# Optimization experiments

Measured on AMD Instinct MI355X. Metric: run time of the kernel, lower is better.

## Reference

```python
import jax, jax.numpy as jnp
import numpy as np

N = 50000      # nodes
E = 800000     # directed edges (before self-loops)
FEAT = 120     # raw node feature dim
TOPO = 8       # topological feature dim
H1, D1 = 8, 8  # conv1: heads, per-head dim
C = 40         # out_channels (classes)
NEG_SLOPE = 0.2


def setup_inputs() -> dict:
    key = jax.random.key(0)
    ks = jax.random.split(key, 10)
    return {
        "x": jax.random.normal(ks[0], (N, FEAT), dtype=jnp.float32),
        "topo": jax.random.normal(ks[1], (N, TOPO), dtype=jnp.float32),
        "edge_index": jax.random.randint(ks[2], (2, E), 0, N, dtype=jnp.int32),
        "W1": jax.random.normal(ks[3], (FEAT + TOPO, H1 * D1), dtype=jnp.float32) * 0.1,
        "a_src1": jax.random.normal(ks[4], (H1, D1), dtype=jnp.float32) * 0.1,
        "a_dst1": jax.random.normal(ks[5], (H1, D1), dtype=jnp.float32) * 0.1,
        "b1": jnp.zeros((H1 * D1,), dtype=jnp.float32),
        "W2": jax.random.normal(ks[6], (H1 * D1, C), dtype=jnp.float32) * 0.1,
        "a_src2": jax.random.normal(ks[7], (1, C), dtype=jnp.float32) * 0.1,
        "a_dst2": jax.random.normal(ks[8], (1, C), dtype=jnp.float32) * 0.1,
        "b2": jnp.zeros((C,), dtype=jnp.float32),
    }


def gat_conv(x, src, dst, W, a_src, a_dst, b, heads, d, concat):
    """PyG-style GATConv (eval mode). src/dst already include self-loops."""
    n = x.shape[0]
    h = (x @ W).reshape(n, heads, d)                      # [N,H,D]
    al_src = jnp.sum(h * a_src[None], axis=-1)            # [N,H]
    al_dst = jnp.sum(h * a_dst[None], axis=-1)            # [N,H]
    e = jax.nn.leaky_relu(al_src[src] + al_dst[dst], NEG_SLOPE)  # [E',H]
    # segment softmax over incoming edges per destination node
    m = jax.ops.segment_max(e, dst, num_segments=n)       # [N,H]
    p = jnp.exp(e - m[dst])                               # [E',H]
    s = jax.ops.segment_sum(p, dst, num_segments=n)       # [N,H]
    alpha = p / s[dst]                                    # [E',H]
    out = jax.ops.segment_sum(alpha[:, :, None] * h[src], dst, num_segments=n)  # [N,H,D]
    if concat:
        return out.reshape(n, heads * d) + b
    return out.mean(axis=1) + b


def reference(x, topo, edge_index, W1, a_src1, a_dst1, b1, W2, a_src2, a_dst2, b2):
    n = x.shape[0]
    loops = jnp.arange(n, dtype=edge_index.dtype)
    src = jnp.concatenate([edge_index[0], loops])
    dst = jnp.concatenate([edge_index[1], loops])
    xin = jnp.concatenate([x, topo], axis=1)              # [N, FEAT+TOPO]
    h = jax.nn.elu(gat_conv(xin, src, dst, W1, a_src1, a_dst1, b1, H1, D1, True))
    out = gat_conv(h, src, dst, W2, a_src2, a_dst2, b2, 1, C, False)
    return jax.nn.log_softmax(out, axis=1)
```

## Files before the change

### kernel.cpp

```cpp
#include <hip/hip_runtime.h>
#include <hip/hip_fp16.h>

#define NN 50000
#define EE 800000
#define NBUCK 196
#define CAP 5120
#define TILEA 2048
#define NBA ((EE + TILEA - 1) / TILEA)
#define NGB 782
#define SRCS_MAX (EE + 8 * NN)

typedef _Float16 half8 __attribute__((ext_vector_type(8)));
typedef float floatx4 __attribute__((ext_vector_type(4)));
typedef float floatx2 __attribute__((ext_vector_type(2)));

__device__ __forceinline__ unsigned char f32_to_fp8(float a) {
    int r = __builtin_amdgcn_cvt_pk_fp8_f32(a, a, 0, false);
    return (unsigned char)(r & 0xff);
}
__device__ __forceinline__ float2 fp8pair_to_f32(unsigned v) {
    floatx2 r = __builtin_amdgcn_cvt_pk_f32_fp8(v, false);
    return make_float2(r[0], r[1]);
}

__global__ void k_prep(const float* __restrict__ W1, const float* __restrict__ W2,
                       _Float16* __restrict__ Bf1, _Float16* __restrict__ Bf2,
                       int* __restrict__ cursor, float* __restrict__ alsrc,
                       float* __restrict__ al2s) {
    int tid = blockIdx.x * 256 + threadIdx.x;
    if (tid < 1024) {
        int kk = tid >> 8, ct = (tid >> 6) & 3, L = tid & 63;
        int k0 = kk * 32 + (L >> 4) * 8, col = ct * 16 + (L & 15);
        half8 v;
        #pragma unroll
        for (int j = 0; j < 8; j++) v[j] = (_Float16)W1[(k0 + j) * 64 + col];
        *(half8*)(Bf1 + ((size_t)((kk * 4 + ct) * 64 + L)) * 8) = v;
    } else if (tid < 1024 + 384) {
        int u = tid - 1024;
        int kk = u / 192, rem = u % 192;
        int ct = rem >> 6, L = rem & 63;
        int k0 = kk * 32 + (L >> 4) * 8, col = ct * 16 + (L & 15);
        half8 v;
        #pragma unroll
        for (int j = 0; j < 8; j++)
            v[j] = (col < 40) ? (_Float16)W2[(k0 + j) * 40 + col] : (_Float16)0.f;
        *(half8*)(Bf2 + ((size_t)((kk * 3 + ct) * 64 + L)) * 8) = v;
    } else {
        int u = tid - 1408;
        if (u < NBUCK) cursor[u] = 0;
        if (u >= 200 && u < 208) alsrc[(size_t)NN * 8 + (u - 200)] = -1e30f;
        if (u == 208) al2s[NN] = -1e30f;
    }
}

__global__ __launch_bounds__(256) void k_fusedAG(
    const int* __restrict__ ei, int* __restrict__ cursor,
    unsigned* __restrict__ bucketData,
    const float* __restrict__ x, const float* __restrict__ topo,
    const _Float16* __restrict__ Bf1,
    const float* __restrict__ a_src, const float* __restrict__ a_dst,
    unsigned char* __restrict__ h1, float* __restrict__ alsrc, float* __restrict__ aldst) {
    if (blockIdx.x < NBA) {
        __shared__ int cnt[NBUCK], base[NBUCK];
        int t = threadIdx.x;
        for (int i = t; i < NBUCK; i += 256) cnt[i] = 0;
        __syncthreads();
        int e0 = blockIdx.x * TILEA;
        int nE = min(TILEA, EE - e0);
        unsigned pk[8]; int bk[8], rk[8];
        int m = 0;
        for (int i = t; i < nE; i += 256) {
            int e = e0 + i;
            int s = ei[e], d = ei[EE + e];
            pk[m] = ((unsigned)d << 16) | (unsigned)s;
            bk[m] = d >> 8;
            rk[m] = atomicAdd(&cnt[bk[m]], 1);
            m++;
        }
        __syncthreads();
        for (int i = t; i < NBUCK; i += 256)
            base[i] = (cnt[i] > 0) ? atomicAdd(&cursor[i], cnt[i]) : 0;
        __syncthreads();
        for (int k = 0; k < m; k++) {
            int pos = base[bk[k]] + rk[k];
            if (pos < CAP) bucketData[(size_t)bk[k] * CAP + pos] = pk[k];
        }
        return;
    }
    int wave = threadIdx.x >> 6, lane = threadIdx.x & 63;
    int row0 = (blockIdx.x - NBA) * 64 + wave * 16;
    if (row0 >= NN) return;
    int g = lane >> 4, li = lane & 15;
    int myrow = row0 + li;
    half8 B[16];
    const half8* bp = (const half8*)Bf1;
    #pragma unroll
    for (int i = 0; i < 16; i++) B[i] = bp[i * 64 + lane];
    floatx4 acc[4] = {{0,0,0,0},{0,0,0,0},{0,0,0,0},{0,0,0,0}};
    #pragma unroll
    for (int kk = 0; kk < 4; kk++) {
        int k0 = kk * 32 + g * 8;
        const float* sp = (k0 == 120) ? (topo + (size_t)myrow * 8)
                                      : (x + (size_t)myrow * 120 + k0);
        float4 u0 = ((const float4*)sp)[0];
        float4 u1 = ((const float4*)sp)[1];
        half8 av;
        av[0] = (_Float16)u0.x; av[1] = (_Float16)u0.y;
        av[2] = (_Float16)u0.z; av[3] = (_Float16)u0.w;
        av[4] = (_Float16)u1.x; av[5] = (_Float16)u1.y;
        av[6] = (_Float16)u1.z; av[7] = (_Float16)u1.w;
        #pragma unroll
        for (int ct = 0; ct < 4; ct++)
            acc[ct] = __builtin_amdgcn_mfma_f32_16x16x32_f16(av, B[kk * 4 + ct], acc[ct], 0, 0, 0);
    }
    #pragma unroll
    for (int ct = 0; ct < 4; ct++)
        #pragma unroll
        for (int r = 0; r < 4; r++)
            h1[(size_t)(row0 + 4 * g + r) * 64 + ct * 16 + li] = f32_to_fp8(acc[ct][r]);
    float ps[4][4], pd[4][4];
    #pragma unroll
    for (int ct = 0; ct < 4; ct++) {
        int head = 2 * ct + (li >> 3), dix = li & 7;
        float asv = a_src[head * 8 + dix];
        float adv = a_dst[head * 8 + dix];
        #pragma unroll
        for (int r = 0; r < 4; r++) {
            ps[ct][r] = acc[ct][r] * asv;
            pd[ct][r] = acc[ct][r] * adv;
        }
    }
    #pragma unroll
    for (int off = 1; off <= 4; off <<= 1)
        #pragma unroll
        for (int ct = 0; ct < 4; ct++)
            #pragma unroll
            for (int r = 0; r < 4; r++) {
                ps[ct][r] += __shfl_xor(ps[ct][r], off, 64);
                pd[ct][r] += __shfl_xor(pd[ct][r], off, 64);
            }
    if ((li & 7) == 0) {
        #pragma unroll
        for (int ct = 0; ct < 4; ct++) {
            int head = 2 * ct + (li >> 3);
            #pragma unroll
            for (int r = 0; r < 4; r++) {
                int row = row0 + 4 * g + r;
                alsrc[row * 8 + head] = ps[ct][r];
                aldst[row * 8 + head] = pd[ct][r];
            }
        }
    }
}

__global__ __launch_bounds__(1024) void k_bucketB(const unsigned* __restrict__ bucketData,
        const int* __restrict__ cursor,
        int2* __restrict__ rowseg, int* __restrict__ srcs) {
    __shared__ int cnt[256], cur[256], sbuf[256], svals[256];
    __shared__ int sorted[CAP + 2048];
    int b = blockIdx.x, t = threadIdx.x;
    int nloc = min(256, NN - b * 256);
    int ecnt = min(cursor[b], CAP);
    size_t inBase = (size_t)b * CAP;
    if (t < 256) {
        int vv = 0;
        if (t < NBUCK) {
            int nl = min(256, NN - t * 256);
            vv = min(cursor[t], CAP) + 8 * nl;
        }
        svals[t] = vv;
    }
    __syncthreads();
    int* a = svals; int* bb = sbuf;
    for (int off = 1; off < 256; off <<= 1) {
        if (t < 256) bb[t] = a[t] + ((t >= off) ? a[t - off] : 0);
        __syncthreads();
        int* tmp = a; a = bb; bb = tmp;
    }
    int outBase = (b == 0) ? 0 : a[b - 1];
    __syncthreads();
    if (t < 256) cnt[t] = (t < nloc) ? 1 : 0;
    __syncthreads();
    for (int i = t; i < ecnt; i += 1024) {
        unsigned u = bucketData[inBase + i];
        atomicAdd(&cnt[(u >> 16) & 255], 1);
    }
    __syncthreads();
    int cv = 0, pcv = 0;
    if (t < 256) {
        cv = cnt[t];
        pcv = (t < nloc) ? ((cv + 7) & ~7) : 0;
        sbuf[t] = pcv;
    }
    __syncthreads();
    a = sbuf; bb = cnt;
    for (int off = 1; off < 256; off <<= 1) {
        if (t < 256) bb[t] = a[t] + ((t >= off) ? a[t - off] : 0);
        __syncthreads();
        int* tmp = a; a = bb; bb = tmp;
    }
    int total = a[255];
    int excl = (t < 256) ? (a[t] - pcv) : 0;
    __syncthreads();
    if (t < nloc) {
        rowseg[b * 256 + t] = make_int2(outBase + excl, outBase + excl + pcv);
        sorted[excl] = b * 256 + t;
        for (int k = cv; k < pcv; k++) sorted[excl + k] = NN;
        cur[t] = excl + 1;
    }
    __syncthreads();
    for (int i = t; i < ecnt; i += 1024) {
        unsigned u = bucketData[inBase + i];
        int ld = (u >> 16) & 255;
        int p = atomicAdd(&cur[ld], 1);
        sorted[p] = (int)(u & 0xffffu);
    }
    __syncthreads();
    for (int i = t; i < total; i += 1024) srcs[outBase + i] = sorted[i];
}

__global__ __launch_bounds__(256) void k_agg1(
    const int2* __restrict__ rowseg, const int* __restrict__ srcs,
    const float* __restrict__ alsrc, const float* __restrict__ aldst,
    const unsigned char* __restrict__ h1, const float* __restrict__ b1,
    __half* __restrict__ hout) {
    int wave = threadIdx.x >> 6;
    int lane = threadIdx.x & 63;
    int d = blockIdx.x * 4 + wave;
    if (d >= NN) return;
    int hs = lane >> 5;
    int cp = lane & 31;
    int hh = cp >> 2;
    float adst = aldst[d * 8 + hh];
    int2 seg = rowseg[d];
    int jb = seg.x, je = seg.y;
    float ssum = 0.f, ax = 0.f, ay = 0.f;
    int sA0 = srcs[jb + hs],     sA1 = srcs[jb + 2 + hs];
    int sA2 = srcs[jb + 4 + hs], sA3 = srcs[jb + 6 + hs];
    for (int j = jb; j < je; j += 8) {
        int s0 = sA0, s1 = sA1, s2 = sA2, s3 = sA3;
        int jn = j + 8;
        if (jn < je) {
            sA0 = srcs[jn + hs];     sA1 = srcs[jn + 2 + hs];
            sA2 = srcs[jn + 4 + hs]; sA3 = srcs[jn + 6 + hs];
        }
        float e0 = alsrc[s0 * 8 + hh] + adst;
        float e1 = alsrc[s1 * 8 + hh] + adst;
        float e2 = alsrc[s2 * 8 + hh] + adst;
        float e3 = alsrc[s3 * 8 + hh] + adst;
        unsigned q0 = *(const unsigned short*)(h1 + (size_t)s0 * 64 + 2 * cp);
        unsigned q1 = *(const unsigned short*)(h1 + (size_t)s1 * 64 + 2 * cp);
        unsigned q2 = *(const unsigned short*)(h1 + (size_t)s2 * 64 + 2 * cp);
        unsigned q3 = *(const unsigned short*)(h1 + (size_t)s3 * 64 + 2 * cp);
        float p0 = __expf(fmaxf(e0, 0.2f * e0));
        float p1 = __expf(fmaxf(e1, 0.2f * e1));
        float p2 = __expf(fmaxf(e2, 0.2f * e2));
        float p3 = __expf(fmaxf(e3, 0.2f * e3));
        float2 f0 = fp8pair_to_f32(q0), f1 = fp8pair_to_f32(q1);
        float2 f2 = fp8pair_to_f32(q2), f3 = fp8pair_to_f32(q3);
        ssum += (p0 + p1) + (p2 + p3);
        ax += p0 * f0.x + p1 * f1.x + p2 * f2.x + p3 * f3.x;
        ay += p0 * f0.y + p1 * f1.y + p2 * f2.y + p3 * f3.y;
    }
    ssum += __shfl_xor(ssum, 32, 64);
    ax += __shfl_xor(ax, 32, 64);
    ay += __shfl_xor(ay, 32, 64);
    if (hs == 0) {
        float2 bv = *(const float2*)(b1 + 2 * cp);
        float inv = 1.f / ssum;
        float vx = ax * inv + bv.x;
        float vy = ay * inv + bv.y;
        vx = (vx > 0.f) ? vx : (__expf(vx) - 1.f);
        vy = (vy > 0.f) ? vy : (__expf(vy) - 1.f);
        *(__half2*)(hout + (size_t)d * 64 + 2 * cp) = __floats2half2_rn(vx, vy);
    }
}

__global__ __launch_bounds__(256) void k_gemm2(
    const __half* __restrict__ hout, const _Float16* __restrict__ Bf2,
    const float* __restrict__ a_src2, const float* __restrict__ a_dst2,
    __half* __restrict__ h2, float* __restrict__ al2s, float* __restrict__ al2d) {
    int wave = threadIdx.x >> 6, lane = threadIdx.x & 63;
    int row0 = blockIdx.x * 64 + wave * 16;
    if (row0 >= NN) return;
    int g = lane >> 4, li = lane & 15;
    int myrow = row0 + li;
    half8 B[6];
    const half8* bp = (const half8*)Bf2;
    #pragma unroll
    for (int i = 0; i < 6; i++) B[i] = bp[i * 64 + lane];
    floatx4 acc[3] = {{0,0,0,0},{0,0,0,0},{0,0,0,0}};
    #pragma unroll
    for (int kk = 0; kk < 2; kk++) {
        int k0 = kk * 32 + g * 8;
        half8 av = *(const half8*)(hout + (size_t)myrow * 64 + k0);
        #pragma unroll
        for (int ct = 0; ct < 3; ct++)
            acc[ct] = __builtin_amdgcn_mfma_f32_16x16x32_f16(av, B[kk * 3 + ct], acc[ct], 0, 0, 0);
    }
    float ts[4] = {0.f, 0.f, 0.f, 0.f}, td[4] = {0.f, 0.f, 0.f, 0.f};
    #pragma unroll
    for (int ct = 0; ct < 3; ct++) {
        int col = ct * 16 + li;
        bool ok = (col < 40);
        float asv = ok ? a_src2[col] : 0.f;
        float adv = ok ? a_dst2[col] : 0.f;
        #pragma unroll
        for (int r = 0; r < 4; r++) {
            ts[r] += acc[ct][r] * asv;
            td[r] += acc[ct][r] * adv;
            if (ok) h2[(size_t)(row0 + 4 * g + r) * 40 + col] = __float2half(acc[ct][r]);
        }
    }
    #pragma unroll
    for (int off = 1; off <= 8; off <<= 1)
        #pragma unroll
        for (int r = 0; r < 4; r++) {
            ts[r] += __shfl_xor(ts[r], off, 64);
            td[r] += __shfl_xor(td[r], off, 64);
        }
    if (li == 0) {
        #pragma unroll
        for (int r = 0; r < 4; r++) {
            int row = row0 + 4 * g + r;
            al2s[row] = ts[r];
            al2d[row] = td[r];
        }
    }
}

__global__ __launch_bounds__(256) void k_agg2(
    const int2* __restrict__ rowseg, const int* __restrict__ srcs,
    const float* __restrict__ al2s, const float* __restrict__ al2d,
    const __half* __restrict__ h2, const float* __restrict__ b2,
    float* __restrict__ out) {
    int wave = threadIdx.x >> 6;
    int lane = threadIdx.x & 63;
    int d = blockIdx.x * 4 + wave;
    if (d >= NN) return;
    int hs = lane >> 5;
    int cp = lane & 31;
    bool act = (cp < 20);
    int cpc = act ? cp : 0;
    float adst = al2d[d];
    int2 seg = rowseg[d];
    int jb = seg.x, je = seg.y;
    float ssum = 0.f, ax = 0.f, ay = 0.f;
    int sA0 = srcs[jb + hs],     sA1 = srcs[jb + 2 + hs];
    int sA2 = srcs[jb + 4 + hs], sA3 = srcs[jb + 6 + hs];
    for (int j = jb; j < je; j += 8) {
        int s0 = sA0, s1 = sA1, s2 = sA2, s3 = sA3;
        int jn = j + 8;
        if (jn < je) {
            sA0 = srcs[jn + hs];     sA1 = srcs[jn + 2 + hs];
            sA2 = srcs[jn + 4 + hs]; sA3 = srcs[jn + 6 + hs];
        }
        float e0 = al2s[s0] + adst;
        float e1 = al2s[s1] + adst;
        float e2 = al2s[s2] + adst;
        float e3 = al2s[s3] + adst;
        __half2 v0 = *(const __half2*)(h2 + (size_t)s0 * 40 + 2 * cpc);
        __half2 v1 = *(const __half2*)(h2 + (size_t)s1 * 40 + 2 * cpc);
        __half2 v2 = *(const __half2*)(h2 + (size_t)s2 * 40 + 2 * cpc);
        __half2 v3 = *(const __half2*)(h2 + (size_t)s3 * 40 + 2 * cpc);
        float p0 = __expf(fmaxf(e0, 0.2f * e0));
        float p1 = __expf(fmaxf(e1, 0.2f * e1));
        float p2 = __expf(fmaxf(e2, 0.2f * e2));
        float p3 = __expf(fmaxf(e3, 0.2f * e3));
        float2 f0 = __half22float2(v0), f1 = __half22float2(v1);
        float2 f2 = __half22float2(v2), f3 = __half22float2(v3);
        ssum += (p0 + p1) + (p2 + p3);
        ax += p0 * f0.x + p1 * f1.x + p2 * f2.x + p3 * f3.x;
        ay += p0 * f0.y + p1 * f1.y + p2 * f2.y + p3 * f3.y;
    }
    ssum += __shfl_xor(ssum, 32, 64);
    ax += __shfl_xor(ax, 32, 64);
    ay += __shfl_xor(ay, 32, 64);
    float inv = 1.f / ssum;
    float2 bv = *(const float2*)(b2 + 2 * cpc);
    float ox = ax * inv + bv.x;
    float oy = ay * inv + bv.y;
    float mo = act ? fmaxf(ox, oy) : -3.0e38f;
    #pragma unroll
    for (int off = 16; off; off >>= 1) mo = fmaxf(mo, __shfl_xor(mo, off, 64));
    float te = act ? (__expf(ox - mo) + __expf(oy - mo)) : 0.f;
    #pragma unroll
    for (int off = 16; off; off >>= 1) te += __shfl_xor(te, off, 64);
    float ls = __logf(te);
    if (act && hs == 0)
        *(float2*)(out + (size_t)d * 40 + 2 * cp) = make_float2(ox - mo - ls, oy - mo - ls);
}

extern "C" void kernel_launch(void* const* d_in, const int* in_sizes, int n_in,
                              void* d_out, int out_size, void* d_ws, size_t ws_size,
                              hipStream_t stream) {
    (void)in_sizes; (void)n_in; (void)out_size; (void)ws_size;
    const float* x    = (const float*)d_in[0];
    const float* topo = (const float*)d_in[1];
    const int*   ei   = (const int*)d_in[2];
    const float* W1   = (const float*)d_in[3];
    const float* as1  = (const float*)d_in[4];
    const float* ad1  = (const float*)d_in[5];
    const float* b1   = (const float*)d_in[6];
    const float* W2   = (const float*)d_in[7];
    const float* as2  = (const float*)d_in[8];
    const float* ad2  = (const float*)d_in[9];
    const float* b2   = (const float*)d_in[10];
    float* out = (float*)d_out;

    char* ws = (char*)d_ws;
    size_t off = 0;
    auto alloc = [&](size_t bytes) {
        void* p = ws + off;
        off += (bytes + 255) / 256 * 256;
        return p;
    };
    int2*          rowseg     = (int2*)alloc((size_t)NN * 8);
    int*           cursor     = (int*)alloc(NBUCK * 4);
    unsigned*      bucketData = (unsigned*)alloc((size_t)NBUCK * CAP * 4);
    int*           srcs       = (int*)alloc((size_t)SRCS_MAX * 4);
    float*         alsrc1     = (float*)alloc((size_t)(NN + 1) * 8 * 4);
    float*         aldst1     = (float*)alloc((size_t)NN * 8 * 4);
    float*         al2s       = (float*)alloc((NN + 1) * 4);
    float*         al2d       = (float*)alloc(NN * 4);
    _Float16*      Bf1        = (_Float16*)alloc(4 * 4 * 64 * 8 * 2);
    _Float16*      Bf2        = (_Float16*)alloc(2 * 3 * 64 * 8 * 2);
    unsigned char* h1         = (unsigned char*)alloc((size_t)(NN + 1) * 64);
    __half*        hout       = (__half*)alloc((size_t)NN * 64 * 2);
    __half*        h2         = (__half*)alloc((size_t)(NN + 1) * 40 * 2);

    k_prep    <<<7,         256,  0, stream>>>(W1, W2, Bf1, Bf2, cursor, alsrc1, al2s);
    k_fusedAG <<<NBA + NGB, 256,  0, stream>>>(ei, cursor, bucketData,
                                               x, topo, Bf1, as1, ad1, h1, alsrc1, aldst1);
    k_bucketB <<<NBUCK,     1024, 0, stream>>>(bucketData, cursor, rowseg, srcs);
    k_agg1    <<<(NN + 3) / 4, 256, 0, stream>>>(rowseg, srcs, alsrc1, aldst1, h1, b1, hout);
    k_gemm2   <<<782,       256,  0, stream>>>(hout, Bf2, as2, ad2, h2, al2s, al2d);
    k_agg2    <<<(NN + 3) / 4, 256, 0, stream>>>(rowseg, srcs, al2s, al2d, h2, b2, out);
}
```

Measured before the change: 172.3 us.

## Fuse layer-2 linear transform into layer-1 aggregation kernel via per-wave MFMA

```diff
diff --git a/kernel.cpp b/kernel.cpp
--- a/kernel.cpp
+++ b/kernel.cpp
@@ -13,6 +13,7 @@
 typedef _Float16 half8 __attribute__((ext_vector_type(8)));
 typedef float floatx4 __attribute__((ext_vector_type(4)));
 typedef float floatx2 __attribute__((ext_vector_type(2)));
+typedef int intx4 __attribute__((ext_vector_type(4)));
 
 __device__ __forceinline__ unsigned char f32_to_fp8(float a) {
     int r = __builtin_amdgcn_cvt_pk_fp8_f32(a, a, 0, false);
@@ -219,11 +220,13 @@
     for (int i = t; i < total; i += 1024) srcs[outBase + i] = sorted[i];
 }
 
-__global__ __launch_bounds__(256) void k_agg1(
+__global__ __launch_bounds__(256) void k_agg1g2(
     const int2* __restrict__ rowseg, const int* __restrict__ srcs,
     const float* __restrict__ alsrc, const float* __restrict__ aldst,
     const unsigned char* __restrict__ h1, const float* __restrict__ b1,
-    __half* __restrict__ hout) {
+    const _Float16* __restrict__ Bf2,
+    const float* __restrict__ a_src2, const float* __restrict__ a_dst2,
+    __half* __restrict__ h2, float* __restrict__ al2s, float* __restrict__ al2d) {
     int wave = threadIdx.x >> 6;
     int lane = threadIdx.x & 63;
     int d = blockIdx.x * 4 + wave;
@@ -265,67 +268,48 @@
     ssum += __shfl_xor(ssum, 32, 64);
     ax += __shfl_xor(ax, 32, 64);
     ay += __shfl_xor(ay, 32, 64);
-    if (hs == 0) {
-        float2 bv = *(const float2*)(b1 + 2 * cp);
-        float inv = 1.f / ssum;
-        float vx = ax * inv + bv.x;
-        float vy = ay * inv + bv.y;
-        vx = (vx > 0.f) ? vx : (__expf(vx) - 1.f);
-        vy = (vy > 0.f) ? vy : (__expf(vy) - 1.f);
-        *(__half2*)(hout + (size_t)d * 64 + 2 * cp) = __floats2half2_rn(vx, vy);
-    }
-}
-
-__global__ __launch_bounds__(256) void k_gemm2(
-    const __half* __restrict__ hout, const _Float16* __restrict__ Bf2,
-    const float* __restrict__ a_src2, const float* __restrict__ a_dst2,
-    __half* __restrict__ h2, float* __restrict__ al2s, float* __restrict__ al2d) {
-    int wave = threadIdx.x >> 6, lane = threadIdx.x & 63;
-    int row0 = blockIdx.x * 64 + wave * 16;
-    if (row0 >= NN) return;
+    float2 bv = *(const float2*)(b1 + 2 * cp);
+    float inv = 1.f / ssum;
+    float vx = ax * inv + bv.x;
+    float vy = ay * inv + bv.y;
+    vx = (vx > 0.f) ? vx : (__expf(vx) - 1.f);
+    vy = (vy > 0.f) ? vy : (__expf(vy) - 1.f);
+    __half2 hp = __floats2half2_rn(vx, vy);
+    int ph = *(int*)&hp;
     int g = lane >> 4, li = lane & 15;
-    int myrow = row0 + li;
-    half8 B[6];
-    const half8* bp = (const half8*)Bf2;
-    #pragma unroll
-    for (int i = 0; i < 6; i++) B[i] = bp[i * 64 + lane];
-    floatx4 acc[3] = {{0,0,0,0},{0,0,0,0},{0,0,0,0}};
-    #pragma unroll
-    for (int kk = 0; kk < 2; kk++) {
-        int k0 = kk * 32 + g * 8;
-        half8 av = *(const half8*)(hout + (size_t)myrow * 64 + k0);
-        #pragma unroll
-        for (int ct = 0; ct < 3; ct++)
-            acc[ct] = __builtin_amdgcn_mfma_f32_16x16x32_f16(av, B[kk * 3 + ct], acc[ct], 0, 0, 0);
-    }
-    float ts[4] = {0.f, 0.f, 0.f, 0.f}, td[4] = {0.f, 0.f, 0.f, 0.f};
-    #pragma unroll
-    for (int ct = 0; ct < 3; ct++) {
-        int col = ct * 16 + li;
-        bool ok = (col < 40);
-        float asv = ok ? a_src2[col] : 0.f;
-        float adv = ok ? a_dst2[col] : 0.f;
-        #pragma unroll
-        for (int r = 0; r < 4; r++) {
-            ts[r] += acc[ct][r] * asv;
-            td[r] += acc[ct][r] * adv;
-            if (ok) h2[(size_t)(row0 + 4 * g + r) * 40 + col] = __float2half(acc[ct][r]);
-        }
-    }
-    #pragma unroll
-    for (int off = 1; off <= 8; off <<= 1)
-        #pragma unroll
-        for (int r = 0; r < 4; r++) {
-            ts[r] += __shfl_xor(ts[r], off, 64);
-            td[r] += __shfl_xor(td[r], off, 64);
-        }
-    if (li == 0) {
-        #pragma unroll
-        for (int r = 0; r < 4; r++) {
-            int row = row0 + 4 * g + r;
-            al2s[row] = ts[r];
-            al2d[row] = td[r];
-        }
+    intx4 i0, i1;
+    #pragma unroll
+    for (int i = 0; i < 4; i++) {
+        i0[i] = __shfl(ph, (g << 2) | i, 64);
+        i1[i] = __shfl(ph, 16 + ((g << 2) | i), 64);
+    }
+    half8 av0 = __builtin_bit_cast(half8, i0);
+    half8 av1 = __builtin_bit_cast(half8, i1);
+    const half8* bp2 = (const half8*)Bf2;
+    floatx4 c0 = {0,0,0,0}, c1 = {0,0,0,0}, c2 = {0,0,0,0};
+    c0 = __builtin_amdgcn_mfma_f32_16x16x32_f16(av0, bp2[0 * 64 + lane], c0, 0, 0, 0);
+    c0 = __builtin_amdgcn_mfma_f32_16x16x32_f16(av1, bp2[3 * 64 + lane], c0, 0, 0, 0);
+    c1 = __builtin_amdgcn_mfma_f32_16x16x32_f16(av0, bp2[1 * 64 + lane], c1, 0, 0, 0);
+    c1 = __builtin_amdgcn_mfma_f32_16x16x32_f16(av1, bp2[4 * 64 + lane], c1, 0, 0, 0);
+    c2 = __builtin_amdgcn_mfma_f32_16x16x32_f16(av0, bp2[2 * 64 + lane], c2, 0, 0, 0);
+    c2 = __builtin_amdgcn_mfma_f32_16x16x32_f16(av1, bp2[5 * 64 + lane], c2, 0, 0, 0);
+    float h20 = c0[0], h21 = c1[0], h22 = c2[0];
+    float as0 = a_src2[li], ad0 = a_dst2[li];
+    float as1 = a_src2[16 + li], ad1 = a_dst2[16 + li];
+    float as2 = (li < 8) ? a_src2[32 + li] : 0.f;
+    float ad2 = (li < 8) ? a_dst2[32 + li] : 0.f;
+    float ts = h20 * as0 + h21 * as1 + h22 * as2;
+    float td = h20 * ad0 + h21 * ad1 + h22 * ad2;
+    #pragma unroll
+    for (int off = 1; off <= 8; off <<= 1) {
+        ts += __shfl_xor(ts, off, 64);
+        td += __shfl_xor(td, off, 64);
+    }
+    if (lane == 0) { al2s[d] = ts; al2d[d] = td; }
+    if (lane < 16) {
+        h2[(size_t)d * 40 + li] = __float2half(h20);
+        h2[(size_t)d * 40 + 16 + li] = __float2half(h21);
+        if (li < 8) h2[(size_t)d * 40 + 32 + li] = __float2half(h22);
     }
 }
 
@@ -426,14 +410,13 @@
     _Float16*      Bf1        = (_Float16*)alloc(4 * 4 * 64 * 8 * 2);
     _Float16*      Bf2        = (_Float16*)alloc(2 * 3 * 64 * 8 * 2);
     unsigned char* h1         = (unsigned char*)alloc((size_t)(NN + 1) * 64);
-    __half*        hout       = (__half*)alloc((size_t)NN * 64 * 2);
     __half*        h2         = (__half*)alloc((size_t)(NN + 1) * 40 * 2);
 
     k_prep    <<<7,         256,  0, stream>>>(W1, W2, Bf1, Bf2, cursor, alsrc1, al2s);
     k_fusedAG <<<NBA + NGB, 256,  0, stream>>>(ei, cursor, bucketData,
                                                x, topo, Bf1, as1, ad1, h1, alsrc1, aldst1);
     k_bucketB <<<NBUCK,     1024, 0, stream>>>(bucketData, cursor, rowseg, srcs);
-    k_agg1    <<<(NN + 3) / 4, 256, 0, stream>>>(rowseg, srcs, alsrc1, aldst1, h1, b1, hout);
-    k_gemm2   <<<782,       256,  0, stream>>>(hout, Bf2, as2, ad2, h2, al2s, al2d);
+    k_agg1g2  <<<(NN + 3) / 4, 256, 0, stream>>>(rowseg, srcs, alsrc1, aldst1, h1, b1,
+                                                 Bf2, as2, ad2, h2, al2s, al2d);
     k_agg2    <<<(NN + 3) / 4, 256, 0, stream>>>(rowseg, srcs, al2s, al2d, h2, b2, out);
 }
```

After: 176.2 us. 2.2% more time.

## Widen per-lane gathers in both aggregation kernels and pad h2 rows to 64

Applied to the files above, without the earlier changes.

```diff
diff --git a/kernel.cpp b/kernel.cpp
--- a/kernel.cpp
+++ b/kernel.cpp
@@ -18,15 +18,20 @@
     int r = __builtin_amdgcn_cvt_pk_fp8_f32(a, a, 0, false);
     return (unsigned char)(r & 0xff);
 }
-__device__ __forceinline__ float2 fp8pair_to_f32(unsigned v) {
+__device__ __forceinline__ float2 fp8pair_lo(unsigned v) {
     floatx2 r = __builtin_amdgcn_cvt_pk_f32_fp8(v, false);
+    return make_float2(r[0], r[1]);
+}
+__device__ __forceinline__ float2 fp8pair_hi(unsigned v) {
+    floatx2 r = __builtin_amdgcn_cvt_pk_f32_fp8(v, true);
     return make_float2(r[0], r[1]);
 }
 
 __global__ void k_prep(const float* __restrict__ W1, const float* __restrict__ W2,
                        _Float16* __restrict__ Bf1, _Float16* __restrict__ Bf2,
                        int* __restrict__ cursor, float* __restrict__ alsrc,
-                       float* __restrict__ al2s) {
+                       float* __restrict__ al2s, unsigned char* __restrict__ h1,
+                       __half* __restrict__ h2p) {
     int tid = blockIdx.x * 256 + threadIdx.x;
     if (tid < 1024) {
         int kk = tid >> 8, ct = (tid >> 6) & 3, L = tid & 63;
@@ -50,6 +55,8 @@
         if (u < NBUCK) cursor[u] = 0;
         if (u >= 200 && u < 208) alsrc[(size_t)NN * 8 + (u - 200)] = -1e30f;
         if (u == 208) al2s[NN] = -1e30f;
+        if (u >= 224 && u < 240) ((unsigned*)(h1 + (size_t)NN * 64))[u - 224] = 0u;
+        if (u >= 240 && u < 272) ((unsigned*)(h2p + (size_t)NN * 64))[u - 240] = 0u;
     }
 }
 
@@ -228,58 +235,62 @@
     int lane = threadIdx.x & 63;
     int d = blockIdx.x * 4 + wave;
     if (d >= NN) return;
-    int hs = lane >> 5;
-    int cp = lane & 31;
-    int hh = cp >> 2;
+    int eh = lane >> 4;
+    int cq = lane & 15;
+    int hh = cq >> 1;
     float adst = aldst[d * 8 + hh];
     int2 seg = rowseg[d];
     int jb = seg.x, je = seg.y;
-    float ssum = 0.f, ax = 0.f, ay = 0.f;
-    int sA0 = srcs[jb + hs],     sA1 = srcs[jb + 2 + hs];
-    int sA2 = srcs[jb + 4 + hs], sA3 = srcs[jb + 6 + hs];
+    float a0 = 0.f, a1 = 0.f, a2 = 0.f, a3 = 0.f, ssum = 0.f;
+    int sA = srcs[jb + eh], sB = srcs[jb + 4 + eh];
     for (int j = jb; j < je; j += 8) {
-        int s0 = sA0, s1 = sA1, s2 = sA2, s3 = sA3;
+        int s0 = sA, s1 = sB;
         int jn = j + 8;
         if (jn < je) {
-            sA0 = srcs[jn + hs];     sA1 = srcs[jn + 2 + hs];
-            sA2 = srcs[jn + 4 + hs]; sA3 = srcs[jn + 6 + hs];
+            sA = srcs[jn + eh]; sB = srcs[jn + 4 + eh];
         }
         float e0 = alsrc[s0 * 8 + hh] + adst;
         float e1 = alsrc[s1 * 8 + hh] + adst;
-        float e2 = alsrc[s2 * 8 + hh] + adst;
-        float e3 = alsrc[s3 * 8 + hh] + adst;
-        unsigned q0 = *(const unsigned short*)(h1 + (size_t)s0 * 64 + 2 * cp);
-        unsigned q1 = *(const unsigned short*)(h1 + (size_t)s1 * 64 + 2 * cp);
-        unsigned q2 = *(const unsigned short*)(h1 + (size_t)s2 * 64 + 2 * cp);
-        unsigned q3 = *(const unsigned short*)(h1 + (size_t)s3 * 64 + 2 * cp);
+        unsigned q0 = *(const unsigned*)(h1 + (size_t)s0 * 64 + 4 * cq);
+        unsigned q1 = *(const unsigned*)(h1 + (size_t)s1 * 64 + 4 * cq);
         float p0 = __expf(fmaxf(e0, 0.2f * e0));
         float p1 = __expf(fmaxf(e1, 0.2f * e1));
-        float p2 = __expf(fmaxf(e2, 0.2f * e2));
-        float p3 = __expf(fmaxf(e3, 0.2f * e3));
-        float2 f0 = fp8pair_to_f32(q0), f1 = fp8pair_to_f32(q1);
-        float2 f2 = fp8pair_to_f32(q2), f3 = fp8pair_to_f32(q3);
-        ssum += (p0 + p1) + (p2 + p3);
-        ax += p0 * f0.x + p1 * f1.x + p2 * f2.x + p3 * f3.x;
-        ay += p0 * f0.y + p1 * f1.y + p2 * f2.y + p3 * f3.y;
-    }
-    ssum += __shfl_xor(ssum, 32, 64);
-    ax += __shfl_xor(ax, 32, 64);
-    ay += __shfl_xor(ay, 32, 64);
-    if (hs == 0) {
-        float2 bv = *(const float2*)(b1 + 2 * cp);
+        float2 f0l = fp8pair_lo(q0), f0h = fp8pair_hi(q0);
+        float2 f1l = fp8pair_lo(q1), f1h = fp8pair_hi(q1);
+        ssum += p0 + p1;
+        a0 += p0 * f0l.x + p1 * f1l.x;
+        a1 += p0 * f0l.y + p1 * f1l.y;
+        a2 += p0 * f0h.x + p1 * f1h.x;
+        a3 += p0 * f0h.y + p1 * f1h.y;
+    }
+    a0 += __shfl_xor(a0, 16, 64); a0 += __shfl_xor(a0, 32, 64);
+    a1 += __shfl_xor(a1, 16, 64); a1 += __shfl_xor(a1, 32, 64);
+    a2 += __shfl_xor(a2, 16, 64); a2 += __shfl_xor(a2, 32, 64);
+    a3 += __shfl_xor(a3, 16, 64); a3 += __shfl_xor(a3, 32, 64);
+    ssum += __shfl_xor(ssum, 16, 64); ssum += __shfl_xor(ssum, 32, 64);
+    if (eh == 0) {
+        float4 bv = ((const float4*)b1)[cq];
         float inv = 1.f / ssum;
-        float vx = ax * inv + bv.x;
-        float vy = ay * inv + bv.y;
-        vx = (vx > 0.f) ? vx : (__expf(vx) - 1.f);
-        vy = (vy > 0.f) ? vy : (__expf(vy) - 1.f);
-        *(__half2*)(hout + (size_t)d * 64 + 2 * cp) = __floats2half2_rn(vx, vy);
+        float v0 = a0 * inv + bv.x;
+        float v1 = a1 * inv + bv.y;
+        float v2 = a2 * inv + bv.z;
+        float v3 = a3 * inv + bv.w;
+        v0 = (v0 > 0.f) ? v0 : (__expf(v0) - 1.f);
+        v1 = (v1 > 0.f) ? v1 : (__expf(v1) - 1.f);
+        v2 = (v2 > 0.f) ? v2 : (__expf(v2) - 1.f);
+        v3 = (v3 > 0.f) ? v3 : (__expf(v3) - 1.f);
+        __half2 h01 = __floats2half2_rn(v0, v1);
+        __half2 h23 = __floats2half2_rn(v2, v3);
+        uint2 pk;
+        pk.x = *(unsigned*)&h01; pk.y = *(unsigned*)&h23;
+        *(uint2*)(hout + (size_t)d * 64 + 4 * cq) = pk;
     }
 }
 
 __global__ __launch_bounds__(256) void k_gemm2(
     const __half* __restrict__ hout, const _Float16* __restrict__ Bf2,
     const float* __restrict__ a_src2, const float* __restrict__ a_dst2,
-    __half* __restrict__ h2, float* __restrict__ al2s, float* __restrict__ al2d) {
+    __half* __restrict__ h2p, float* __restrict__ al2s, float* __restrict__ al2d) {
     int wave = threadIdx.x >> 6, lane = threadIdx.x & 63;
     int row0 = blockIdx.x * 64 + wave * 16;
     if (row0 >= NN) return;
@@ -309,9 +320,12 @@
         for (int r = 0; r < 4; r++) {
             ts[r] += acc[ct][r] * asv;
             td[r] += acc[ct][r] * adv;
-            if (ok) h2[(size_t)(row0 + 4 * g + r) * 40 + col] = __float2half(acc[ct][r]);
-        }
-    }
+            h2p[(size_t)(row0 + 4 * g + r) * 64 + col] = __float2half(acc[ct][r]);
+        }
+    }
+    #pragma unroll
+    for (int r = 0; r < 4; r++)
+        h2p[(size_t)(row0 + 4 * g + r) * 64 + 48 + li] = (__half)0.f;
     #pragma unroll
     for (int off = 1; off <= 8; off <<= 1)
         #pragma unroll
@@ -332,63 +346,64 @@
 __global__ __launch_bounds__(256) void k_agg2(
     const int2* __restrict__ rowseg, const int* __restrict__ srcs,
     const float* __restrict__ al2s, const float* __restrict__ al2d,
-    const __half* __restrict__ h2, const float* __restrict__ b2,
+    const __half* __restrict__ h2p, const float* __restrict__ b2,
     float* __restrict__ out) {
     int wave = threadIdx.x >> 6;
     int lane = threadIdx.x & 63;
     int d = blockIdx.x * 4 + wave;
     if (d >= NN) return;
-    int hs = lane >> 5;
-    int cp = lane & 31;
-    bool act = (cp < 20);
-    int cpc = act ? cp : 0;
+    int eh = lane >> 4;
+    int cq = lane & 15;
+    bool act = (cq < 10);
     float adst = al2d[d];
     int2 seg = rowseg[d];
     int jb = seg.x, je = seg.y;
-    float ssum = 0.f, ax = 0.f, ay = 0.f;
-    int sA0 = srcs[jb + hs],     sA1 = srcs[jb + 2 + hs];
-    int sA2 = srcs[jb + 4 + hs], sA3 = srcs[jb + 6 + hs];
+    float a0 = 0.f, a1 = 0.f, a2 = 0.f, a3 = 0.f, ssum = 0.f;
+    int sA = srcs[jb + eh], sB = srcs[jb + 4 + eh];
     for (int j = jb; j < je; j += 8) {
-        int s0 = sA0, s1 = sA1, s2 = sA2, s3 = sA3;
+        int s0 = sA, s1 = sB;
         int jn = j + 8;
         if (jn < je) {
-            sA0 = srcs[jn + hs];     sA1 = srcs[jn + 2 + hs];
-            sA2 = srcs[jn + 4 + hs]; sA3 = srcs[jn + 6 + hs];
+            sA = srcs[jn + eh]; sB = srcs[jn + 4 + eh];
         }
         float e0 = al2s[s0] + adst;
         float e1 = al2s[s1] + adst;
-        float e2 = al2s[s2] + adst;
-        float e3 = al2s[s3] + adst;
-        __half2 v0 = *(const __half2*)(h2 + (size_t)s0 * 40 + 2 * cpc);
-        __half2 v1 = *(const __half2*)(h2 + (size_t)s1 * 40 + 2 * cpc);
-        __half2 v2 = *(const __half2*)(h2 + (size_t)s2 * 40 + 2 * cpc);
-        __half2 v3 = *(const __half2*)(h2 + (size_t)s3 * 40 + 2 * cpc);
+        uint2 q0 = *(const uint2*)(h2p + (size_t)s0 * 64 + 4 * cq);
+        uint2 q1 = *(const uint2*)(h2p + (size_t)s1 * 64 + 4 * cq);
         float p0 = __expf(fmaxf(e0, 0.2f * e0));
         float p1 = __expf(fmaxf(e1, 0.2f * e1));
-        float p2 = __expf(fmaxf(e2, 0.2f * e2));
-        float p3 = __expf(fmaxf(e3, 0.2f * e3));
-        float2 f0 = __half22float2(v0), f1 = __half22float2(v1);
-        float2 f2 = __half22float2(v2), f3 = __half22float2(v3);
-        ssum += (p0 + p1) + (p2 + p3);
-        ax += p0 * f0.x + p1 * f1.x + p2 * f2.x + p3 * f3.x;
-        ay += p0 * f0.y + p1 * f1.y + p2 * f2.y + p3 * f3.y;
-    }
-    ssum += __shfl_xor(ssum, 32, 64);
-    ax += __shfl_xor(ax, 32, 64);
-    ay += __shfl_xor(ay, 32, 64);
+        float2 f0l = __half22float2(*(__half2*)&q0.x);
+        float2 f0h = __half22float2(*(__half2*)&q0.y);
+        float2 f1l = __half22float2(*(__half2*)&q1.x);
+        float2 f1h = __half22float2(*(__half2*)&q1.y);
+        ssum += p0 + p1;
+        a0 += p0 * f0l.x + p1 * f1l.x;
+        a1 += p0 * f0l.y + p1 * f1l.y;
+        a2 += p0 * f0h.x + p1 * f1h.x;
+        a3 += p0 * f0h.y + p1 * f1h.y;
+    }
+    a0 += __shfl_xor(a0, 16, 64); a0 += __shfl_xor(a0, 32, 64);
+    a1 += __shfl_xor(a1, 16, 64); a1 += __shfl_xor(a1, 32, 64);
+    a2 += __shfl_xor(a2, 16, 64); a2 += __shfl_xor(a2, 32, 64);
+    a3 += __shfl_xor(a3, 16, 64); a3 += __shfl_xor(a3, 32, 64);
+    ssum += __shfl_xor(ssum, 16, 64); ssum += __shfl_xor(ssum, 32, 64);
     float inv = 1.f / ssum;
-    float2 bv = *(const float2*)(b2 + 2 * cpc);
-    float ox = ax * inv + bv.x;
-    float oy = ay * inv + bv.y;
-    float mo = act ? fmaxf(ox, oy) : -3.0e38f;
-    #pragma unroll
-    for (int off = 16; off; off >>= 1) mo = fmaxf(mo, __shfl_xor(mo, off, 64));
-    float te = act ? (__expf(ox - mo) + __expf(oy - mo)) : 0.f;
-    #pragma unroll
-    for (int off = 16; off; off >>= 1) te += __shfl_xor(te, off, 64);
+    float4 bv = act ? ((const float4*)b2)[cq] : make_float4(0.f, 0.f, 0.f, 0.f);
+    float o0 = a0 * inv + bv.x;
+    float o1 = a1 * inv + bv.y;
+    float o2 = a2 * inv + bv.z;
+    float o3 = a3 * inv + bv.w;
+    float mo = act ? fmaxf(fmaxf(o0, o1), fmaxf(o2, o3)) : -3.0e38f;
+    #pragma unroll
+    for (int off = 1; off <= 8; off <<= 1) mo = fmaxf(mo, __shfl_xor(mo, off, 64));
+    float te = act ? (__expf(o0 - mo) + __expf(o1 - mo) + __expf(o2 - mo) + __expf(o3 - mo)) : 0.f;
+    #pragma unroll
+    for (int off = 1; off <= 8; off <<= 1) te += __shfl_xor(te, off, 64);
     float ls = __logf(te);
-    if (act && hs == 0)
-        *(float2*)(out + (size_t)d * 40 + 2 * cp) = make_float2(ox - mo - ls, oy - mo - ls);
+    if (act && eh == 0) {
+        float4 ov = make_float4(o0 - mo - ls, o1 - mo - ls, o2 - mo - ls, o3 - mo - ls);
+        *(float4*)(out + (size_t)d * 40 + 4 * cq) = ov;
+    }
 }
 
 extern "C" void kernel_launch(void* const* d_in, const int* in_sizes, int n_in,
@@ -427,13 +442,13 @@
     _Float16*      Bf2        = (_Float16*)alloc(2 * 3 * 64 * 8 * 2);
     unsigned char* h1         = (unsigned char*)alloc((size_t)(NN + 1) * 64);
     __half*        hout       = (__half*)alloc((size_t)NN * 64 * 2);
-    __half*        h2         = (__half*)alloc((size_t)(NN + 1) * 40 * 2);
-
-    k_prep    <<<7,         256,  0, stream>>>(W1, W2, Bf1, Bf2, cursor, alsrc1, al2s);
+    __half*        h2p        = (__half*)alloc((size_t)(NN + 1) * 64 * 2);
+
+    k_prep    <<<7,         256,  0, stream>>>(W1, W2, Bf1, Bf2, cursor, alsrc1, al2s, h1, h2p);
     k_fusedAG <<<NBA + NGB, 256,  0, stream>>>(ei, cursor, bucketData,
                                                x, topo, Bf1, as1, ad1, h1, alsrc1, aldst1);
     k_bucketB <<<NBUCK,     1024, 0, stream>>>(bucketData, cursor, rowseg, srcs);
     k_agg1    <<<(NN + 3) / 4, 256, 0, stream>>>(rowseg, srcs, alsrc1, aldst1, h1, b1, hout);
-    k_gemm2   <<<782,       256,  0, stream>>>(hout, Bf2, as2, ad2, h2, al2s, al2d);
-    k_agg2    <<<(NN + 3) / 4, 256, 0, stream>>>(rowseg, srcs, al2s, al2d, h2, b2, out);
-}
+    k_gemm2   <<<782,       256,  0, stream>>>(hout, Bf2, as2, ad2, h2p, al2s, al2d);
+    k_agg2    <<<(NN + 3) / 4, 256, 0, stream>>>(rowseg, srcs, al2s, al2d, h2p, b2, out);
+}
```

New measurement: 171.1 us. No clear change (-0.7%).
